# Kernel optimization log

Hardware: AMD Instinct MI355X
Metric: run time of the kernel (lower is better)

The kernel has to match this reference:

```python
import jax, jax.numpy as jnp
import numpy as np

RADIUS = 0.12   # init_kwargs radius
NSAMPLE = 32    # init_kwargs nsample
USE_XYZ = True  # init_kwargs use_xyz


def ball_query(xyz, new_xyz, radius, nsample):
    """xyz: (B,N,3), new_xyz: (B,M,3) -> idx (B,M,nsample) int32.
    PointNet++ semantics: first `nsample` points (in index order) within
    `radius` of each query; slots past the count are padded with the first
    found index."""
    B, N, _ = xyz.shape
    # squared distances (B, M, N) -- the dominant intermediate
    d2 = jnp.sum((new_xyz[:, :, None, :] - xyz[:, None, :, :]) ** 2, axis=-1)
    mask = d2 < radius * radius
    # score so that earlier in-ball indices have higher score; out-of-ball = 0
    score = jnp.where(mask, (N - jnp.arange(N, dtype=jnp.int32)), 0)
    _, idx = jax.lax.top_k(score, nsample)            # (B, M, nsample)
    valid = jnp.take_along_axis(mask, idx, axis=-1)   # which slots are real hits
    idx = jnp.where(valid, idx, idx[..., :1])         # pad with first found index
    return idx


def group_points(feat, idx):
    """feat: (B,C,N), idx: (B,M,S) -> (B,C,M,S) gather along N."""
    B, C, N = feat.shape
    M, S = idx.shape[1], idx.shape[2]
    idx_flat = jnp.broadcast_to(idx.reshape(B, 1, M * S), (B, C, M * S))
    out = jnp.take_along_axis(feat, idx_flat, axis=2)
    return out.reshape(B, C, M, S)


def setup_inputs() -> dict:
    key = jax.random.key(0)
    k1, k2 = jax.random.split(key)
    B, N, M, C = 4, 8192, 4096, 64
    xyz = jax.random.uniform(k1, (B, N, 3), dtype=jnp.float32)  # points in unit cube
    new_xyz = xyz[:, :M, :]                                      # FPS-like subset of points
    features = jax.random.normal(k2, (B, C, N), dtype=jnp.float32)
    return {"xyz": xyz, "new_xyz": new_xyz, "features": features}


def reference(xyz, new_xyz, features):
    idx = ball_query(xyz, new_xyz, RADIUS, NSAMPLE)             # (B,M,S)
    xyz_t = jnp.transpose(xyz, (0, 2, 1))                        # (B,3,N)
    grouped_xyz = group_points(xyz_t, idx)                       # (B,3,M,S)
    grouped_xyz = grouped_xyz - jnp.transpose(new_xyz, (0, 2, 1))[..., None]
    grouped_feat = group_points(features, idx)                   # (B,C,M,S)
    if USE_XYZ:
        new_features = jnp.concatenate([grouped_xyz, grouped_feat], axis=1)
    else:
        new_features = grouped_feat
    return new_features  # (B, 3+C, M, S)
```

## Files before the change

### kernel.cpp

```cpp
#include <hip/hip_runtime.h>
#include <cstdint>
#include <cstddef>

#define BB 4
#define NN 8192
#define MM 4096
#define CC 64
#define SS 32
#define CH 67
#define NC 512
#define RMARG 0.1201f

__device__ __constant__ float kRR = (float)(0.12 * 0.12);

__device__ __forceinline__ int cell_of(float x, float y, float z) {
    const int ix = min((int)(x * 8.0f), 7);
    const int iy = min((int)(y * 8.0f), 7);
    const int iz = min((int)(z * 8.0f), 7);
    return (ix << 6) + (iy << 3) + iz;
}

__global__ __launch_bounds__(1024) void k_prep(
    const float* __restrict__ xyz,
    const float* __restrict__ feat,
    float* __restrict__ ft,
    int* __restrict__ cellStart,
    float4* __restrict__ pk)
{
    __shared__ __align__(16) char smem[64 * 65 * sizeof(float)];
    const int blk = (int)blockIdx.x;
    const int tid = (int)threadIdx.x;

    if (blk < BB) {
        int* sm  = (int*)smem;
        int* cur = sm + NC;
        const int b = blk;

        if (tid < NC) sm[tid] = 0;
        __syncthreads();

        float xs[8], ys[8], zs[8];
        int cl[8];
        const float* __restrict__ xb = xyz + (size_t)b * NN * 3;
        #pragma unroll
        for (int k = 0; k < 8; ++k) {
            const int n = (k << 10) + tid;
            xs[k] = xb[n * 3 + 0];
            ys[k] = xb[n * 3 + 1];
            zs[k] = xb[n * 3 + 2];
            cl[k] = cell_of(xs[k], ys[k], zs[k]);
            atomicAdd(&sm[cl[k]], 1);
        }
        __syncthreads();

        int v = 0;
        if (tid < NC) v = sm[tid];
        for (int d = 1; d < NC; d <<= 1) {
            int u = 0;
            if (tid < NC && tid >= d) u = sm[tid - d];
            __syncthreads();
            if (tid < NC) sm[tid] += u;
            __syncthreads();
        }
        if (tid < NC) {
            const int inc = sm[tid];
            cellStart[b * (NC + 1) + tid + 1] = inc;
            cur[tid] = inc - v;
            if (tid == 0) cellStart[b * (NC + 1)] = 0;
        }
        __syncthreads();

        #pragma unroll
        for (int k = 0; k < 8; ++k) {
            const int n = (k << 10) + tid;
            const int pos = atomicAdd(&cur[cl[k]], 1);
            pk[b * NN + pos] = make_float4(xs[k], ys[k], zs[k], __int_as_float(n));
        }
    } else {
        float (*tile)[65] = (float(*)[65])smem;
        const int blk2 = blk - BB;
        const int b = blk2 / (NN / 64);
        const int n0 = (blk2 % (NN / 64)) * 64;
        const int tn = tid & 63;
        const int q = tid >> 6;
        const float* __restrict__ fb = feat + (size_t)b * CC * NN;
        #pragma unroll
        for (int k = 0; k < 4; ++k) {
            const int c = (q << 2) + k;
            tile[tn][c] = fb[(size_t)c * NN + n0 + tn];
        }
        __syncthreads();
        float* fo = ft + ((size_t)b * NN + n0) * CC;
        #pragma unroll
        for (int k = 0; k < 4; ++k) {
            const int rn = (q << 2) + k;
            fo[(size_t)rn * CC + tn] = tile[rn][tn];
        }
    }
}

__global__ __launch_bounds__(256) void qg_grid_kernel(
    const float4* __restrict__ pk,
    const int* __restrict__ cellStart,
    const float* __restrict__ ft,
    const float* __restrict__ xyz,
    const float* __restrict__ new_xyz,
    float* __restrict__ out)
{
    __shared__ unsigned int bm[4][NN / 32];
    __shared__ int slots_sm[4][SS];

    const int tid = (int)threadIdx.x;
    const int lane = tid & 63;
    const int w = tid >> 6;
    const int wave = (int)blockIdx.x * 4 + w;
    const int b = wave >> 12;
    const int m = wave & (MM - 1);

    unsigned int* __restrict__ bitmap = bm[w];
    int* __restrict__ slot = slots_sm[w];

    #pragma unroll
    for (int k = 0; k < 4; ++k) bitmap[(k << 6) + lane] = 0u;

    const float* __restrict__ xb = xyz + (size_t)b * NN * 3;
    const size_t qoff = ((size_t)b * MM + m) * 3;
    const float cx = new_xyz[qoff + 0];
    const float cy = new_xyz[qoff + 1];
    const float cz = new_xyz[qoff + 2];
    const float rr = kRR;

    const int x0 = max(0, (int)((cx - RMARG) * 8.0f));
    const int x1 = min(7, (int)((cx + RMARG) * 8.0f));
    const int y0 = max(0, (int)((cy - RMARG) * 8.0f));
    const int y1 = min(7, (int)((cy + RMARG) * 8.0f));
    const int z0 = max(0, (int)((cz - RMARG) * 8.0f));
    const int z1 = min(7, (int)((cz + RMARG) * 8.0f));

    const int* __restrict__ cs = cellStart + b * (NC + 1);
    const float4* __restrict__ pb = pk + b * NN;

    for (int ix = x0; ix <= x1; ++ix) {
        for (int iy = y0; iy <= y1; ++iy) {
            const int cbase = (ix << 6) + (iy << 3);
            const int beg = cs[cbase + z0];
            const int end = cs[cbase + z1 + 1];
            for (int off = beg; off < end; off += 64) {
                const int a = off + lane;
                const bool act = a < end;
                const float4 v = pb[act ? a : beg];
                const float dx = __fsub_rn(v.x, cx);
                const float dy = __fsub_rn(v.y, cy);
                const float dz = __fsub_rn(v.z, cz);
                const float d2 = __fadd_rn(__fadd_rn(__fmul_rn(dx, dx), __fmul_rn(dy, dy)),
                                           __fmul_rn(dz, dz));
                if (act && d2 < rr) {
                    const int n = __float_as_int(v.w);
                    atomicOr(&bitmap[n >> 5], 1u << (n & 31));
                }
            }
        }
    }

    const uint4 wv = *reinterpret_cast<const uint4*>(&bitmap[lane << 2]);
    const int pc = __popc(wv.x) + __popc(wv.y) + __popc(wv.z) + __popc(wv.w);
    int incl = pc;
    #pragma unroll
    for (int d = 1; d < 64; d <<= 1) {
        const int t = __shfl_up(incl, d);
        if (lane >= d) incl += t;
    }
    const int K = __shfl(incl, 63);
    int r = incl - pc;
    if (r < SS) {
        const int base = lane << 7;
        unsigned int mw0 = wv.x, mw1 = wv.y, mw2 = wv.z, mw3 = wv.w;
        while (mw0 && r < SS) { slot[r++] = base +  0 + __builtin_ctz(mw0); mw0 &= mw0 - 1; }
        while (mw1 && r < SS) { slot[r++] = base + 32 + __builtin_ctz(mw1); mw1 &= mw1 - 1; }
        while (mw2 && r < SS) { slot[r++] = base + 64 + __builtin_ctz(mw2); mw2 &= mw2 - 1; }
        while (mw3 && r < SS) { slot[r++] = base + 96 + __builtin_ctz(mw3); mw3 &= mw3 - 1; }
    }

    const int s = lane & 31;
    const int h = lane >> 5;
    const int Kc = (K < SS) ? K : SS;
    int n_of;
    if (Kc == 0) n_of = 0;
    else n_of = (s < Kc) ? slot[s] : slot[0];

    const size_t obase = ((size_t)b * CH) * (size_t)(MM * SS) + (size_t)m * SS + s;

    if (h == 0) {
        const float* xr = xb + (size_t)n_of * 3;
        out[obase + 0 * (size_t)(MM * SS)] = __fsub_rn(xr[0], cx);
        out[obase + 1 * (size_t)(MM * SS)] = __fsub_rn(xr[1], cy);
        out[obase + 2 * (size_t)(MM * SS)] = __fsub_rn(xr[2], cz);
    }
    const float4* fr4 = (const float4*)(ft + ((size_t)b * NN + n_of) * CC + (h << 5));
    float4 f[8];
    #pragma unroll
    for (int j = 0; j < 8; ++j) f[j] = fr4[j];
    #pragma unroll
    for (int j = 0; j < 8; ++j) {
        const size_t cb = obase + (size_t)(3 + (h << 5) + (j << 2)) * (size_t)(MM * SS);
        out[cb + 0 * (size_t)(MM * SS)] = f[j].x;
        out[cb + 1 * (size_t)(MM * SS)] = f[j].y;
        out[cb + 2 * (size_t)(MM * SS)] = f[j].z;
        out[cb + 3 * (size_t)(MM * SS)] = f[j].w;
    }
}

__global__ __launch_bounds__(256) void qg_fused_kernel(
    const float* __restrict__ xyz, const float* __restrict__ new_xyz,
    const float* __restrict__ feat, float* __restrict__ out)
{
    const int wave = (int)((blockIdx.x * blockDim.x + threadIdx.x) >> 6);
    const int lane = (int)(threadIdx.x & 63);
    const int b = wave / MM;
    const int m = wave % MM;

    const float* __restrict__ xb = xyz + (size_t)b * NN * 3;
    const size_t qoff = ((size_t)b * MM + m) * 3;
    const float cx = new_xyz[qoff + 0];
    const float cy = new_xyz[qoff + 1];
    const float cz = new_xyz[qoff + 2];
    const float rr = kRR;

    int my_nb = -1;
    int cnt = 0;

    for (int base = 0; base < NN; base += 512) {
        float px[8], py[8], pz[8];
        #pragma unroll
        for (int k = 0; k < 8; ++k) {
            const int i = base + (k << 6) + lane;
            px[k] = xb[i * 3 + 0]; py[k] = xb[i * 3 + 1]; pz[k] = xb[i * 3 + 2];
        }
        #pragma unroll
        for (int k = 0; k < 8; ++k) {
            const float dx = __fsub_rn(px[k], cx);
            const float dy = __fsub_rn(py[k], cy);
            const float dz = __fsub_rn(pz[k], cz);
            const float d2 = __fadd_rn(__fadd_rn(__fmul_rn(dx, dx), __fmul_rn(dy, dy)),
                                       __fmul_rn(dz, dz));
            const bool hit = d2 < rr;
            const unsigned long long mask = __ballot(hit);
            const int pc = __popcll(mask);
            if (pc) {
                const int rank = cnt + (int)__popcll(mask & ((1ull << lane) - 1ull));
                const int addr = (hit && rank < 63) ? rank : 63;
                const int recv = __builtin_amdgcn_ds_permute(addr << 2,
                                                             base + (k << 6) + lane);
                if (lane >= cnt && lane < SS && (lane - cnt) < pc) my_nb = recv;
                cnt += pc;
                if (cnt >= SS) break;
            }
        }
        if (cnt >= SS) break;
    }

    int first = __shfl(my_nb, 0);
    if (first < 0) first = 0;
    if (lane < SS && my_nb < 0) my_nb = first;
    const int n_of = __shfl(my_nb, lane & 31);

    const int s = lane & 31;
    const int h = lane >> 5;
    const size_t obase = ((size_t)b * CH) * (size_t)(MM * SS) + (size_t)m * SS + s;
    const float* __restrict__ fb = feat + (size_t)b * CC * NN;
    #pragma unroll 2
    for (int cc = 0; cc < CH + 1; cc += 2) {
        const int c = cc + h;
        if (c < CH) {
            float v;
            if (c < 3) {
                const float center = (c == 0) ? cx : (c == 1) ? cy : cz;
                v = __fsub_rn(xb[(size_t)n_of * 3 + c], center);
            } else {
                v = fb[(size_t)(c - 3) * NN + n_of];
            }
            out[obase + (size_t)c * (size_t)(MM * SS)] = v;
        }
    }
}

extern "C" void kernel_launch(void* const* d_in, const int* in_sizes, int n_in,
                              void* d_out, int out_size, void* d_ws, size_t ws_size,
                              hipStream_t stream) {
    const float* xyz     = (const float*)d_in[0];
    const float* new_xyz = (const float*)d_in[1];
    const float* feat    = (const float*)d_in[2];
    float* out = (float*)d_out;

    const size_t ft_b = (size_t)BB * NN * CC * sizeof(float);
    float*  ft     = (float*)d_ws;
    int*    cellSt = (int*)((char*)d_ws + ft_b);
    char*   after  = (char*)(cellSt + BB * (NC + 1));
    float4* pk     = (float4*)(((uintptr_t)after + 15) & ~(uintptr_t)15);
    const size_t need = ((char*)(pk + BB * NN) - (char*)d_ws);

    if (ws_size >= need) {
        k_prep<<<BB + BB * (NN / 64), 1024, 0, stream>>>(xyz, feat, ft, cellSt, pk);
        qg_grid_kernel<<<(BB * MM) / 4, 256, 0, stream>>>(pk, cellSt, ft, xyz,
                                                          new_xyz, out);
    } else {
        qg_fused_kernel<<<(BB * MM) / 4, 256, 0, stream>>>(xyz, new_xyz, feat, out);
    }
}
```

Measured before the change: 60.86 us.

## Sort queries by grid cell and preload cell ranges per lane

After: 60.58 us. About the same (-0.5%).

```diff
diff --git a/kernel.cpp b/kernel.cpp
--- a/kernel.cpp
+++ b/kernel.cpp
@@ -22,9 +22,11 @@
 
 __global__ __launch_bounds__(1024) void k_prep(
     const float* __restrict__ xyz,
+    const float* __restrict__ new_xyz,
     const float* __restrict__ feat,
     float* __restrict__ ft,
     int* __restrict__ cellStart,
+    int* __restrict__ qperm,
     float4* __restrict__ pk)
 {
     __shared__ __align__(16) char smem[64 * 65 * sizeof(float)];
@@ -76,6 +78,39 @@
             const int pos = atomicAdd(&cur[cl[k]], 1);
             pk[b * NN + pos] = make_float4(xs[k], ys[k], zs[k], __int_as_float(n));
         }
+        __syncthreads();
+
+        if (tid < NC) sm[tid] = 0;
+        __syncthreads();
+        int qcl[4];
+        const float* __restrict__ qb = new_xyz + (size_t)b * MM * 3;
+        #pragma unroll
+        for (int k = 0; k < 4; ++k) {
+            const int qm = (k << 10) + tid;
+            const float qx = qb[qm * 3 + 0];
+            const float qy = qb[qm * 3 + 1];
+            const float qz = qb[qm * 3 + 2];
+            qcl[k] = cell_of(qx, qy, qz);
+            atomicAdd(&sm[qcl[k]], 1);
+        }
+        __syncthreads();
+        int qv = 0;
+        if (tid < NC) qv = sm[tid];
+        for (int d = 1; d < NC; d <<= 1) {
+            int u = 0;
+            if (tid < NC && tid >= d) u = sm[tid - d];
+            __syncthreads();
+            if (tid < NC) sm[tid] += u;
+            __syncthreads();
+        }
+        if (tid < NC) cur[tid] = sm[tid] - qv;
+        __syncthreads();
+        #pragma unroll
+        for (int k = 0; k < 4; ++k) {
+            const int qm = (k << 10) + tid;
+            const int pos = atomicAdd(&cur[qcl[k]], 1);
+            qperm[b * MM + pos] = qm;
+        }
     } else {
         float (*tile)[65] = (float(*)[65])smem;
         const int blk2 = blk - BB;
@@ -102,6 +137,7 @@
 __global__ __launch_bounds__(256) void qg_grid_kernel(
     const float4* __restrict__ pk,
     const int* __restrict__ cellStart,
+    const int* __restrict__ qperm,
     const float* __restrict__ ft,
     const float* __restrict__ xyz,
     const float* __restrict__ new_xyz,
@@ -115,7 +151,8 @@
     const int w = tid >> 6;
     const int wave = (int)blockIdx.x * 4 + w;
     const int b = wave >> 12;
-    const int m = wave & (MM - 1);
+    const int msort = wave & (MM - 1);
+    const int m = qperm[b * MM + msort];
 
     unsigned int* __restrict__ bitmap = bm[w];
     int* __restrict__ slot = slots_sm[w];
@@ -140,24 +177,32 @@
     const int* __restrict__ cs = cellStart + b * (NC + 1);
     const float4* __restrict__ pb = pk + b * NN;
 
-    for (int ix = x0; ix <= x1; ++ix) {
-        for (int iy = y0; iy <= y1; ++iy) {
-            const int cbase = (ix << 6) + (iy << 3);
-            const int beg = cs[cbase + z0];
-            const int end = cs[cbase + z1 + 1];
-            for (int off = beg; off < end; off += 64) {
-                const int a = off + lane;
-                const bool act = a < end;
-                const float4 v = pb[act ? a : beg];
-                const float dx = __fsub_rn(v.x, cx);
-                const float dy = __fsub_rn(v.y, cy);
-                const float dz = __fsub_rn(v.z, cz);
-                const float d2 = __fadd_rn(__fadd_rn(__fmul_rn(dx, dx), __fmul_rn(dy, dy)),
-                                           __fmul_rn(dz, dz));
-                if (act && d2 < rr) {
-                    const int n = __float_as_int(v.w);
-                    atomicOr(&bitmap[n >> 5], 1u << (n & 31));
-                }
+    const int ny = y1 - y0 + 1;
+    const int npair = (x1 - x0 + 1) * ny;
+    int begL = 0, endL = 0;
+    if (lane < npair) {
+        const int px = lane / ny;
+        const int py = lane - px * ny;
+        const int cb2 = ((x0 + px) << 6) + ((y0 + py) << 3);
+        begL = cs[cb2 + z0];
+        endL = cs[cb2 + z1 + 1];
+    }
+
+    for (int p = 0; p < npair; ++p) {
+        const int beg = __shfl(begL, p);
+        const int end = __shfl(endL, p);
+        for (int off = beg; off < end; off += 64) {
+            const int a = off + lane;
+            const bool act = a < end;
+            const float4 v = pb[act ? a : beg];
+            const float dx = __fsub_rn(v.x, cx);
+            const float dy = __fsub_rn(v.y, cy);
+            const float dz = __fsub_rn(v.z, cz);
+            const float d2 = __fadd_rn(__fadd_rn(__fmul_rn(dx, dx), __fmul_rn(dy, dy)),
+                                       __fmul_rn(dz, dz));
+            if (act && d2 < rr) {
+                const int n = __float_as_int(v.w);
+                atomicOr(&bitmap[n >> 5], 1u << (n & 31));
             }
         }
     }
@@ -295,14 +340,16 @@
     const size_t ft_b = (size_t)BB * NN * CC * sizeof(float);
     float*  ft     = (float*)d_ws;
     int*    cellSt = (int*)((char*)d_ws + ft_b);
-    char*   after  = (char*)(cellSt + BB * (NC + 1));
+    int*    qperm  = cellSt + BB * (NC + 1);
+    char*   after  = (char*)(qperm + BB * MM);
     float4* pk     = (float4*)(((uintptr_t)after + 15) & ~(uintptr_t)15);
     const size_t need = ((char*)(pk + BB * NN) - (char*)d_ws);
 
     if (ws_size >= need) {
-        k_prep<<<BB + BB * (NN / 64), 1024, 0, stream>>>(xyz, feat, ft, cellSt, pk);
-        qg_grid_kernel<<<(BB * MM) / 4, 256, 0, stream>>>(pk, cellSt, ft, xyz,
-                                                          new_xyz, out);
+        k_prep<<<BB + BB * (NN / 64), 1024, 0, stream>>>(xyz, new_xyz, feat, ft,
+                                                         cellSt, qperm, pk);
+        qg_grid_kernel<<<(BB * MM) / 4, 256, 0, stream>>>(pk, cellSt, qperm, ft,
+                                                          xyz, new_xyz, out);
     } else {
         qg_fused_kernel<<<(BB * MM) / 4, 256, 0, stream>>>(xyz, new_xyz, feat, out);
     }
```
